# Performance work log

Hardware: AMD Instinct MI355X
Metric: run time of the kernel (lower is better)

The kernel has to match this reference:

```python
import jax, jax.numpy as jnp
import numpy as np
import math

B, S, E, H = 2, 2048, 1024, 16
D = E // H

def setup_inputs() -> dict:
    key = jax.random.key(0)
    ks = jax.random.split(key, 12)
    f = lambda k, shp: jax.random.normal(k, shp, dtype=jnp.float32)
    inp = {
        'Q': f(ks[0], (B, S, E)),
        'K': f(ks[1], (B, S, E)),
        'V': f(ks[2], (B, S, E)),
        # torch nn.Linear stores weight as [out, in]; y = x @ W.T + b
        'Wq': f(ks[3], (E, E)) * 0.02, 'bq': f(ks[4], (E,)) * 0.02,
        'Wk': f(ks[5], (E, E)) * 0.02, 'bk': f(ks[6], (E,)) * 0.02,
        'Wv': f(ks[7], (E, E)) * 0.02, 'bv': f(ks[8], (E,)) * 0.02,
        'Wo': f(ks[9], (E, E)) * 0.02, 'bo': f(ks[10], (E,)) * 0.02,
        # causal mask, broadcast over batch and heads: [1,1,S,S]
        'mask': jnp.tril(jnp.ones((S, S), dtype=jnp.int32))[None, None],
    }
    return inp

def reference(Q, K, V, Wq, bq, Wk, bk, Wv, bv, Wo, bo, mask):
    scale = 1.0 / math.sqrt(D)
    def proj(x, W, b):  # [B,S,E] -> [B,H,S,D]
        return (x @ W.T + b).reshape(B, S, H, D).transpose(0, 2, 1, 3)
    q = proj(Q, Wq, bq)
    k = proj(K, Wk, bk)
    v = proj(V, Wv, bv)
    scores = jnp.einsum('bhqd,bhkd->bhqk', q, k) * scale  # [B,H,S,S]
    scores = jnp.where(mask == 0, jnp.float32(-jnp.inf), scores)
    probs = jax.nn.softmax(scores, axis=-1)
    # dropout is identity in eval mode (deterministic reference)
    attn = jnp.einsum('bhqk,bhkd->bhqd', probs, v)
    attn = attn.transpose(0, 2, 1, 3).reshape(B, S, E)
    return attn @ Wo.T + bo
```

## Files before the change

### kernel.cpp

```cpp
#include <hip/hip_runtime.h>
#include <hip/hip_bf16.h>
#include <stdint.h>
#include <stddef.h>

#define S_LEN 2048
#define EMB   1024
#define NH    16
#define DH    64
#define BB    2
#define QBLK  64
#define NQT   (S_LEN / QBLK)

typedef short s16;
typedef __attribute__((ext_vector_type(8))) short bf16x8;
typedef __attribute__((ext_vector_type(4))) short s16x4;
typedef __attribute__((ext_vector_type(4))) float f32x4;

__device__ __forceinline__ float b2f(s16 x) {
  union { unsigned u; float f; } t;
  t.u = ((unsigned)(unsigned short)x) << 16;
  return t.f;
}
__device__ __forceinline__ s16 f2b(float f) {
  union { float f; unsigned u; } t;
  t.f = f;
  unsigned u = t.u;
  unsigned r = (u + 0x7FFFu + ((u >> 16) & 1u)) >> 16;
  return (s16)r;
}

__device__ __forceinline__ void gld16(const void* g, void* l) {
  __builtin_amdgcn_global_load_lds(
      (const __attribute__((address_space(1))) void*)g,
      (__attribute__((address_space(3))) void*)l, 16, 0, 0);
}
__device__ __forceinline__ void drain_and_barrier() {
  asm volatile("s_waitcnt vmcnt(0)" ::: "memory");
  __builtin_amdgcn_s_barrier();
}

struct CvtArgs { const float* src[11]; s16* dst[11]; int n[11]; };

__global__ __launch_bounds__(256)
void convert_in(CvtArgs a) {
  const int t = blockIdx.z;
  const int n = a.n[t];
  const int base = blockIdx.x * 2048 + threadIdx.x * 8;
  if (base >= n) return;
  const float* s = a.src[t] + base;
  float4 v0 = *(const float4*)s;
  float4 v1 = *(const float4*)(s + 4);
  bf16x8 o;
  o[0] = f2b(v0.x); o[1] = f2b(v0.y); o[2] = f2b(v0.z); o[3] = f2b(v0.w);
  o[4] = f2b(v1.x); o[5] = f2b(v1.y); o[6] = f2b(v1.z); o[7] = f2b(v1.w);
  *(bf16x8*)(a.dst[t] + base) = o;
}

struct GemmSet { const s16* X; const s16* W; const s16* Bv; s16* Y; float* Yf; int mode; };
struct GemmArgs { GemmSet t[3]; };

__global__ __launch_bounds__(256, 2)
void gemm_bt(GemmArgs args) {
  constexpr int K = EMB;
  constexpr int BK = 64;
  __shared__ __align__(16) s16 As[128][BK];
  __shared__ __align__(16) s16 Ws[128][BK];

  GemmSet p = args.t[blockIdx.z];
  const int tid  = threadIdx.x;
  const int lane = tid & 63;
  const int wave = tid >> 6;
  const int wr = wave >> 1, wc = wave & 1;
  const int l16 = lane & 15, lh = lane >> 4;
  const int brow = blockIdx.y * 128;
  const int bcol = blockIdx.x * 128;

  f32x4 acc[4][4] = {};

  for (int kt = 0; kt < K; kt += BK) {
#pragma unroll
    for (int r = 0; r < 4; ++r) {
      int cc = r * 256 + tid;
      int row = cc >> 3, col8 = (cc & 7) << 3;
      gld16(p.X + (size_t)(brow + row) * K + kt + col8, &As[row][col8]);
    }
#pragma unroll
    for (int r = 0; r < 4; ++r) {
      int cc = r * 256 + tid;
      int row = cc >> 3, col8 = (cc & 7) << 3;
      gld16(p.W + (size_t)(bcol + row) * K + kt + col8, &Ws[row][col8]);
    }
    __syncthreads();
#pragma unroll
    for (int kk = 0; kk < BK; kk += 32) {
      bf16x8 af[4], bfr[4];
#pragma unroll
      for (int i = 0; i < 4; ++i)
        af[i] = *(const bf16x8*)&As[wr * 64 + i * 16 + l16][kk + lh * 8];
#pragma unroll
      for (int j = 0; j < 4; ++j)
        bfr[j] = *(const bf16x8*)&Ws[wc * 64 + j * 16 + l16][kk + lh * 8];
#pragma unroll
      for (int i = 0; i < 4; ++i)
#pragma unroll
        for (int j = 0; j < 4; ++j)
          acc[i][j] = __builtin_amdgcn_mfma_f32_16x16x32_bf16(af[i], bfr[j], acc[i][j], 0, 0, 0);
    }
    __syncthreads();
  }

  const int mode = p.mode;
  float bv[4];
#pragma unroll
  for (int j = 0; j < 4; ++j) bv[j] = b2f(p.Bv[bcol + wc * 64 + j * 16 + l16]);
#pragma unroll
  for (int i = 0; i < 4; ++i) {
    int row0 = brow + wr * 64 + i * 16 + lh * 4;
#pragma unroll
    for (int j = 0; j < 4; ++j) {
      int col = bcol + wc * 64 + j * 16 + l16;
      if (mode == 2) {
        int bq = row0 >> 11, s0 = row0 & (S_LEN - 1);
        int hh = col >> 6, dd = col & 63;
        s16x4 pk;
#pragma unroll
        for (int t = 0; t < 4; ++t) pk[t] = f2b(acc[i][j][t] + bv[j]);
        *(s16x4*)&p.Y[(((size_t)bq * NH + hh) * DH + dd) * S_LEN + s0] = pk;
      } else {
#pragma unroll
        for (int t = 0; t < 4; ++t) {
          float v = acc[i][j][t] + bv[j];
          int r = row0 + t;
          if (mode == 0) {
            int bq = r >> 11, s = r & (S_LEN - 1);
            int hh = col >> 6, dd = col & 63;
            p.Y[((((size_t)bq * NH + hh) * S_LEN + s) << 6) + dd] = f2b(v);
          } else {
            p.Yf[(size_t)r * EMB + col] = v;
          }
        }
      }
    }
  }
}

__global__ __launch_bounds__(256, 3)
void attn_fwd(const s16* __restrict__ Qb, const s16* __restrict__ Kb,
              const s16* __restrict__ Vtb, s16* __restrict__ Ob) {
  __shared__ __align__(16) s16 Ks[2][4096];
  __shared__ __align__(16) s16 Vt[2][4096];
  __shared__ __align__(16) s16 Ps[4][16][68];

  const int tid  = threadIdx.x;
  const int lane = tid & 63;
  const int wave = tid >> 6;
  const int l16 = lane & 15, lh = lane >> 4;

  const int bid = blockIdx.x;
  const int xcd = bid & 7, slot = bid >> 3;
  const int bh = xcd * 4 + (slot >> 5);
  const int qi = (NQT - 1) - (slot & 31);
  const int qb = qi * QBLK;
  const int b = bh >> 4, h = bh & 15;

  const s16* Qp = Qb + (size_t)bh * S_LEN * DH;
  const s16* Kp = Kb + (size_t)bh * S_LEN * DH;
  const s16* Vp = Vtb + (size_t)bh * DH * S_LEN;

  auto stage_kv = [&](int kb, int bf) {
#pragma unroll
    for (int r = 0; r < 2; ++r) {
      int u = r * 256 + tid;
      int row = ((u >> 7) << 4) + (u & 15);
      int ch  = (((u >> 6) & 1) << 2) + ((u >> 4) & 3);
      gld16(Kp + (size_t)(kb + row) * DH + (ch << 3), &Ks[bf][(size_t)u * 8]);
    }
#pragma unroll
    for (int r = 0; r < 2; ++r) {
      int u = r * 256 + tid;
      int dv = ((u >> 7) << 4) + (u & 15);
      int ch = (((u >> 6) & 1) << 2) + ((u >> 4) & 3);
      gld16(Vp + (size_t)dv * S_LEN + kb + (ch << 3), &Vt[bf][(size_t)u * 8]);
    }
  };

  bf16x8 qf[2];
#pragma unroll
  for (int kk = 0; kk < 2; ++kk)
    qf[kk] = *(const bf16x8*)(Qp + (size_t)(qb + wave * 16 + l16) * DH + kk * 32 + lh * 8);

  stage_kv(0, 0);
  drain_and_barrier();

  float mrow[4], lrow[4];
  f32x4 accO[4] = {};
#pragma unroll
  for (int i = 0; i < 4; ++i) { mrow[i] = -1e30f; lrow[i] = 0.f; }

  int c = 0;
  for (int t = 0; t <= qi; ++t) {
    const int kb = t * QBLK;
    if (t < qi) stage_kv(kb + QBLK, c ^ 1);

    f32x4 sc[4] = {};
    __builtin_amdgcn_s_setprio(1);
#pragma unroll
    for (int kk = 0; kk < 2; ++kk) {
#pragma unroll
      for (int j = 0; j < 4; ++j) {
        bf16x8 kf = *(const bf16x8*)&Ks[c][(((j * 2 + kk) * 64) + lane) * 8];
        sc[j] = __builtin_amdgcn_mfma_f32_16x16x32_bf16(qf[kk], kf, sc[j], 0, 0, 0);
      }
    }
    __builtin_amdgcn_s_setprio(0);

    const bool diag = (t == qi);
    float pm[4];
#pragma unroll
    for (int i = 0; i < 4; ++i) {
#pragma unroll
      for (int j = 0; j < 4; ++j) {
        float s = sc[j][i] * 0.125f;
        if (diag && (kb + j * 16 + l16 > qb + wave * 16 + lh * 4 + i)) s = -1e30f;
        sc[j][i] = s;
      }
      pm[i] = fmaxf(fmaxf(sc[0][i], sc[1][i]), fmaxf(sc[2][i], sc[3][i]));
    }
#pragma unroll
    for (int d = 1; d < 16; d <<= 1)
#pragma unroll
      for (int i = 0; i < 4; ++i) pm[i] = fmaxf(pm[i], __shfl_xor(pm[i], d));
#pragma unroll
    for (int i = 0; i < 4; ++i) {
      float mnew = fmaxf(mrow[i], pm[i]);
      float corr = __expf(mrow[i] - mnew);
      mrow[i] = mnew;
      float rs = 0.f;
#pragma unroll
      for (int j = 0; j < 4; ++j) { float pv = __expf(sc[j][i] - mnew); sc[j][i] = pv; rs += pv; }
#pragma unroll
      for (int d = 1; d < 16; d <<= 1) rs += __shfl_xor(rs, d);
      lrow[i] = lrow[i] * corr + rs;
#pragma unroll
      for (int dc = 0; dc < 4; ++dc) accO[dc][i] *= corr;
    }

#pragma unroll
    for (int i = 0; i < 4; ++i)
#pragma unroll
      for (int j = 0; j < 4; ++j)
        Ps[wave][lh * 4 + i][j * 16 + l16] = f2b(sc[j][i]);

    bf16x8 pf[2];
#pragma unroll
    for (int kk = 0; kk < 2; ++kk) {
      const s16* pp = &Ps[wave][l16][kk * 32 + lh * 8];
      s16x4 lo = *(const s16x4*)pp;
      s16x4 hi = *(const s16x4*)(pp + 4);
      pf[kk] = __builtin_shufflevector(lo, hi, 0, 1, 2, 3, 4, 5, 6, 7);
    }
    __builtin_amdgcn_s_setprio(1);
#pragma unroll
    for (int kk = 0; kk < 2; ++kk) {
#pragma unroll
      for (int dc = 0; dc < 4; ++dc) {
        bf16x8 vf = *(const bf16x8*)&Vt[c][(((dc * 2 + kk) * 64) + lane) * 8];
        accO[dc] = __builtin_amdgcn_mfma_f32_16x16x32_bf16(pf[kk], vf, accO[dc], 0, 0, 0);
      }
    }
    __builtin_amdgcn_s_setprio(0);
    drain_and_barrier();
    c ^= 1;
  }

#pragma unroll
  for (int i = 0; i < 4; ++i) {
    float inv = 1.f / lrow[i];
    int srow = qb + wave * 16 + lh * 4 + i;
    size_t rowbase = ((size_t)b * S_LEN + srow) * EMB + h * DH;
#pragma unroll
    for (int dc = 0; dc < 4; ++dc)
      Ob[rowbase + dc * 16 + l16] = f2b(accO[dc][i] * inv);
  }
}

extern "C" void kernel_launch(void* const* d_in, const int* in_sizes, int n_in,
                              void* d_out, int out_size, void* d_ws, size_t ws_size,
                              hipStream_t stream) {
  const size_t NQ = (size_t)BB * S_LEN * EMB;
  const size_t NW = (size_t)EMB * EMB;
  const size_t NB2 = EMB;

  s16* Qc  = (s16*)d_ws;
  s16* Kc  = Qc + NQ;
  s16* Vc  = Kc + NQ;
  s16* Wqc = Vc + NQ;
  s16* Wkc = Wqc + NW;
  s16* Wvc = Wkc + NW;
  s16* Woc = Wvc + NW;
  s16* bqc = Woc + NW;
  s16* bkc = bqc + NB2;
  s16* bvc = bkc + NB2;
  s16* boc = bvc + NB2;
  s16* qw  = boc + NB2;
  s16* kw  = qw + NQ;
  s16* vw  = kw + NQ;
  s16* aw  = Qc;

  CvtArgs ca;
  const int srcmap[11] = {0, 1, 2, 3, 5, 7, 9, 4, 6, 8, 10};
  s16* dsts[11] = {Qc, Kc, Vc, Wqc, Wkc, Wvc, Woc, bqc, bkc, bvc, boc};
  for (int i = 0; i < 11; ++i) {
    ca.src[i] = (const float*)d_in[srcmap[i]];
    ca.dst[i] = dsts[i];
    ca.n[i]   = in_sizes[srcmap[i]];
  }
  convert_in<<<dim3(2048, 1, 11), 256, 0, stream>>>(ca);

  GemmArgs qkv;
  qkv.t[0] = {Qc, Wqc, bqc, qw, nullptr, 0};
  qkv.t[1] = {Kc, Wkc, bkc, kw, nullptr, 0};
  qkv.t[2] = {Vc, Wvc, bvc, vw, nullptr, 2};
  gemm_bt<<<dim3(8, 32, 3), 256, 0, stream>>>(qkv);

  attn_fwd<<<dim3(1024, 1), 256, 0, stream>>>(qw, kw, vw, aw);

  GemmArgs og;
  og.t[0] = {aw, Woc, boc, nullptr, (float*)d_out, 1};
  og.t[1] = og.t[0];
  og.t[2] = og.t[0];
  gemm_bt<<<dim3(8, 32, 1), 256, 0, stream>>>(og);
}
```

Before: 282.5 us.

## Transpose attention MFMA operands, keep P in registers, pair causal tiles per block

The attention kernel swaps the MFMA operand order (K as A, Q as B), so each lane holds a query column. The softmax reduction then needs only two cross-lane shuffles, and P is packed straight into bf16 MFMA fragments with v_cvt_pk_bf16_f32 instead of going through an LDS scratch tile. K is staged with a permuted row order to match the new fragment layout. Each block now handles a short and a long causal q-tile pair to balance work, with half as many blocks and occupancy hint 2. The 1/sqrt(D) scale is folded into the Q projection epilogue, which rounds the scaled value to bf16 earlier.

```diff
diff --git a/kernel.cpp b/kernel.cpp
--- a/kernel.cpp
+++ b/kernel.cpp
@@ -27,6 +27,11 @@
   unsigned u = t.u;
   unsigned r = (u + 0x7FFFu + ((u >> 16) & 1u)) >> 16;
   return (s16)r;
+}
+__device__ __forceinline__ unsigned cvtpk(float lo, float hi) {
+  unsigned r;
+  asm("v_cvt_pk_bf16_f32 %0, %1, %2" : "=v"(r) : "v"(lo), "v"(hi));
+  return r;
 }
 
 __device__ __forceinline__ void gld16(const void* g, void* l) {
@@ -56,7 +61,7 @@
   *(bf16x8*)(a.dst[t] + base) = o;
 }
 
-struct GemmSet { const s16* X; const s16* W; const s16* Bv; s16* Y; float* Yf; int mode; };
+struct GemmSet { const s16* X; const s16* W; const s16* Bv; s16* Y; float* Yf; float scale; int mode; };
 struct GemmArgs { GemmSet t[3]; };
 
 __global__ __launch_bounds__(256, 2)
@@ -110,6 +115,7 @@
   }
 
   const int mode = p.mode;
+  const float sc = p.scale;
   float bv[4];
 #pragma unroll
   for (int j = 0; j < 4; ++j) bv[j] = b2f(p.Bv[bcol + wc * 64 + j * 16 + l16]);
@@ -124,12 +130,12 @@
         int hh = col >> 6, dd = col & 63;
         s16x4 pk;
 #pragma unroll
-        for (int t = 0; t < 4; ++t) pk[t] = f2b(acc[i][j][t] + bv[j]);
+        for (int t = 0; t < 4; ++t) pk[t] = f2b((acc[i][j][t] + bv[j]) * sc);
         *(s16x4*)&p.Y[(((size_t)bq * NH + hh) * DH + dd) * S_LEN + s0] = pk;
       } else {
 #pragma unroll
         for (int t = 0; t < 4; ++t) {
-          float v = acc[i][j][t] + bv[j];
+          float v = (acc[i][j][t] + bv[j]) * sc;
           int r = row0 + t;
           if (mode == 0) {
             int bq = r >> 11, s = r & (S_LEN - 1);
@@ -144,12 +150,11 @@
   }
 }
 
-__global__ __launch_bounds__(256, 3)
+__global__ __launch_bounds__(256, 2)
 void attn_fwd(const s16* __restrict__ Qb, const s16* __restrict__ Kb,
               const s16* __restrict__ Vtb, s16* __restrict__ Ob) {
   __shared__ __align__(16) s16 Ks[2][4096];
   __shared__ __align__(16) s16 Vt[2][4096];
-  __shared__ __align__(16) s16 Ps[4][16][68];
 
   const int tid  = threadIdx.x;
   const int lane = tid & 63;
@@ -158,9 +163,8 @@
 
   const int bid = blockIdx.x;
   const int xcd = bid & 7, slot = bid >> 3;
-  const int bh = xcd * 4 + (slot >> 5);
-  const int qi = (NQT - 1) - (slot & 31);
-  const int qb = qi * QBLK;
+  const int bh = xcd * 4 + (slot >> 4);
+  const int qp = slot & 15;
   const int b = bh >> 4, h = bh & 15;
 
   const s16* Qp = Qb + (size_t)bh * S_LEN * DH;
@@ -171,9 +175,9 @@
 #pragma unroll
     for (int r = 0; r < 2; ++r) {
       int u = r * 256 + tid;
-      int row = ((u >> 7) << 4) + (u & 15);
-      int ch  = (((u >> 6) & 1) << 2) + ((u >> 4) & 3);
-      gld16(Kp + (size_t)(kb + row) * DH + (ch << 3), &Ks[bf][(size_t)u * 8]);
+      int rowp = ((u >> 8) & 1) * 32 + ((u >> 2) & 3) * 8 + ((u >> 7) & 1) * 4 + (u & 3);
+      int ch   = (((u >> 6) & 1) << 2) + ((u >> 4) & 3);
+      gld16(Kp + (size_t)(kb + rowp) * DH + (ch << 3), &Ks[bf][(size_t)u * 8]);
     }
 #pragma unroll
     for (int r = 0; r < 2; ++r) {
@@ -184,103 +188,105 @@
     }
   };
 
-  bf16x8 qf[2];
-#pragma unroll
-  for (int kk = 0; kk < 2; ++kk)
-    qf[kk] = *(const bf16x8*)(Qp + (size_t)(qb + wave * 16 + l16) * DH + kk * 32 + lh * 8);
-
-  stage_kv(0, 0);
-  drain_and_barrier();
-
-  float mrow[4], lrow[4];
-  f32x4 accO[4] = {};
-#pragma unroll
-  for (int i = 0; i < 4; ++i) { mrow[i] = -1e30f; lrow[i] = 0.f; }
-
-  int c = 0;
-  for (int t = 0; t <= qi; ++t) {
-    const int kb = t * QBLK;
-    if (t < qi) stage_kv(kb + QBLK, c ^ 1);
-
-    f32x4 sc[4] = {};
-    __builtin_amdgcn_s_setprio(1);
-#pragma unroll
-    for (int kk = 0; kk < 2; ++kk) {
-#pragma unroll
-      for (int j = 0; j < 4; ++j) {
-        bf16x8 kf = *(const bf16x8*)&Ks[c][(((j * 2 + kk) * 64) + lane) * 8];
-        sc[j] = __builtin_amdgcn_mfma_f32_16x16x32_bf16(qf[kk], kf, sc[j], 0, 0, 0);
+  for (int sel = 0; sel < 2; ++sel) {
+    const int qi = sel ? (NQT - 1 - qp) : qp;
+    const int qb = qi * QBLK;
+    const int q_glob = qb + wave * 16 + l16;
+
+    bf16x8 qf[2];
+#pragma unroll
+    for (int kk = 0; kk < 2; ++kk)
+      qf[kk] = *(const bf16x8*)(Qp + (size_t)q_glob * DH + kk * 32 + lh * 8);
+
+    stage_kv(0, 0);
+    drain_and_barrier();
+
+    float m = -1e30f, lsum = 0.f;
+    f32x4 accO[4] = {};
+
+    int c = 0;
+    for (int t = 0; t <= qi; ++t) {
+      const int kb = t * QBLK;
+      if (t < qi) stage_kv(kb + QBLK, c ^ 1);
+
+      f32x4 sc[4] = {};
+      __builtin_amdgcn_s_setprio(1);
+#pragma unroll
+      for (int kk = 0; kk < 2; ++kk) {
+#pragma unroll
+        for (int jb = 0; jb < 4; ++jb) {
+          bf16x8 kf = *(const bf16x8*)&Ks[c][(((jb * 2 + kk) * 64) + lane) * 8];
+          sc[jb] = __builtin_amdgcn_mfma_f32_16x16x32_bf16(kf, qf[kk], sc[jb], 0, 0, 0);
+        }
       }
-    }
-    __builtin_amdgcn_s_setprio(0);
-
-    const bool diag = (t == qi);
-    float pm[4];
-#pragma unroll
-    for (int i = 0; i < 4; ++i) {
-#pragma unroll
-      for (int j = 0; j < 4; ++j) {
-        float s = sc[j][i] * 0.125f;
-        if (diag && (kb + j * 16 + l16 > qb + wave * 16 + lh * 4 + i)) s = -1e30f;
-        sc[j][i] = s;
+      __builtin_amdgcn_s_setprio(0);
+
+      const int rel = q_glob - kb;
+      float pm = -1e30f;
+#pragma unroll
+      for (int jb = 0; jb < 4; ++jb)
+#pragma unroll
+        for (int r = 0; r < 4; ++r) {
+          int koff = ((jb >> 1) << 5) + (lh << 3) + ((jb & 1) << 2) + r;
+          float s = (koff <= rel) ? sc[jb][r] : -1e30f;
+          sc[jb][r] = s;
+          pm = fmaxf(pm, s);
+        }
+      pm = fmaxf(pm, __shfl_xor(pm, 16));
+      pm = fmaxf(pm, __shfl_xor(pm, 32));
+
+      float mnew = fmaxf(m, pm);
+      float corr = __expf(m - mnew);
+      m = mnew;
+      float rs = 0.f;
+#pragma unroll
+      for (int jb = 0; jb < 4; ++jb)
+#pragma unroll
+        for (int r = 0; r < 4; ++r) {
+          float pv = __expf(sc[jb][r] - mnew);
+          sc[jb][r] = pv;
+          rs += pv;
+        }
+      rs += __shfl_xor(rs, 16);
+      rs += __shfl_xor(rs, 32);
+      lsum = lsum * corr + rs;
+#pragma unroll
+      for (int dc = 0; dc < 4; ++dc) accO[dc] *= corr;
+
+      bf16x8 pf[2];
+#pragma unroll
+      for (int kk = 0; kk < 2; ++kk) {
+        union { unsigned u[4]; bf16x8 v; } pk;
+        pk.u[0] = cvtpk(sc[2 * kk][0], sc[2 * kk][1]);
+        pk.u[1] = cvtpk(sc[2 * kk][2], sc[2 * kk][3]);
+        pk.u[2] = cvtpk(sc[2 * kk + 1][0], sc[2 * kk + 1][1]);
+        pk.u[3] = cvtpk(sc[2 * kk + 1][2], sc[2 * kk + 1][3]);
+        pf[kk] = pk.v;
       }
-      pm[i] = fmaxf(fmaxf(sc[0][i], sc[1][i]), fmaxf(sc[2][i], sc[3][i]));
-    }
-#pragma unroll
-    for (int d = 1; d < 16; d <<= 1)
-#pragma unroll
-      for (int i = 0; i < 4; ++i) pm[i] = fmaxf(pm[i], __shfl_xor(pm[i], d));
-#pragma unroll
-    for (int i = 0; i < 4; ++i) {
-      float mnew = fmaxf(mrow[i], pm[i]);
-      float corr = __expf(mrow[i] - mnew);
-      mrow[i] = mnew;
-      float rs = 0.f;
-#pragma unroll
-      for (int j = 0; j < 4; ++j) { float pv = __expf(sc[j][i] - mnew); sc[j][i] = pv; rs += pv; }
-#pragma unroll
-      for (int d = 1; d < 16; d <<= 1) rs += __shfl_xor(rs, d);
-      lrow[i] = lrow[i] * corr + rs;
-#pragma unroll
-      for (int dc = 0; dc < 4; ++dc) accO[dc][i] *= corr;
-    }
-
-#pragma unroll
-    for (int i = 0; i < 4; ++i)
-#pragma unroll
-      for (int j = 0; j < 4; ++j)
-        Ps[wave][lh * 4 + i][j * 16 + l16] = f2b(sc[j][i]);
-
-    bf16x8 pf[2];
-#pragma unroll
-    for (int kk = 0; kk < 2; ++kk) {
-      const s16* pp = &Ps[wave][l16][kk * 32 + lh * 8];
-      s16x4 lo = *(const s16x4*)pp;
-      s16x4 hi = *(const s16x4*)(pp + 4);
-      pf[kk] = __builtin_shufflevector(lo, hi, 0, 1, 2, 3, 4, 5, 6, 7);
-    }
-    __builtin_amdgcn_s_setprio(1);
-#pragma unroll
-    for (int kk = 0; kk < 2; ++kk) {
-#pragma unroll
-      for (int dc = 0; dc < 4; ++dc) {
-        bf16x8 vf = *(const bf16x8*)&Vt[c][(((dc * 2 + kk) * 64) + lane) * 8];
-        accO[dc] = __builtin_amdgcn_mfma_f32_16x16x32_bf16(pf[kk], vf, accO[dc], 0, 0, 0);
+
+      __builtin_amdgcn_s_setprio(1);
+#pragma unroll
+      for (int kk = 0; kk < 2; ++kk) {
+#pragma unroll
+        for (int dc = 0; dc < 4; ++dc) {
+          bf16x8 vf = *(const bf16x8*)&Vt[c][(((dc * 2 + kk) * 64) + lane) * 8];
+          accO[dc] = __builtin_amdgcn_mfma_f32_16x16x32_bf16(vf, pf[kk], accO[dc], 0, 0, 0);
+        }
       }
-    }
-    __builtin_amdgcn_s_setprio(0);
-    drain_and_barrier();
-    c ^= 1;
-  }
-
-#pragma unroll
-  for (int i = 0; i < 4; ++i) {
-    float inv = 1.f / lrow[i];
-    int srow = qb + wave * 16 + lh * 4 + i;
-    size_t rowbase = ((size_t)b * S_LEN + srow) * EMB + h * DH;
-#pragma unroll
-    for (int dc = 0; dc < 4; ++dc)
-      Ob[rowbase + dc * 16 + l16] = f2b(accO[dc][i] * inv);
+      __builtin_amdgcn_s_setprio(0);
+      drain_and_barrier();
+      c ^= 1;
+    }
+
+    float inv = 1.f / lsum;
+    size_t rowbase = ((size_t)b * S_LEN + q_glob) * EMB + h * DH;
+#pragma unroll
+    for (int dc = 0; dc < 4; ++dc) {
+      s16x4 pk;
+#pragma unroll
+      for (int r = 0; r < 4; ++r) pk[r] = f2b(accO[dc][r] * inv);
+      *(s16x4*)&Ob[rowbase + dc * 16 + lh * 4] = pk;
+    }
   }
 }
 
@@ -318,15 +324,15 @@
   convert_in<<<dim3(2048, 1, 11), 256, 0, stream>>>(ca);
 
   GemmArgs qkv;
-  qkv.t[0] = {Qc, Wqc, bqc, qw, nullptr, 0};
-  qkv.t[1] = {Kc, Wkc, bkc, kw, nullptr, 0};
-  qkv.t[2] = {Vc, Wvc, bvc, vw, nullptr, 2};
+  qkv.t[0] = {Qc, Wqc, bqc, qw, nullptr, 0.125f, 0};
+  qkv.t[1] = {Kc, Wkc, bkc, kw, nullptr, 1.0f, 0};
+  qkv.t[2] = {Vc, Wvc, bvc, vw, nullptr, 1.0f, 2};
   gemm_bt<<<dim3(8, 32, 3), 256, 0, stream>>>(qkv);
 
-  attn_fwd<<<dim3(1024, 1), 256, 0, stream>>>(qw, kw, vw, aw);
+  attn_fwd<<<dim3(512, 1), 256, 0, stream>>>(qw, kw, vw, aw);
 
   GemmArgs og;
-  og.t[0] = {aw, Woc, boc, nullptr, (float*)d_out, 1};
+  og.t[0] = {aw, Woc, boc, nullptr, (float*)d_out, 1.0f, 1};
   og.t[1] = og.t[0];
   og.t[2] = og.t[0];
   gemm_bt<<<dim3(8, 32, 1), 256, 0, stream>>>(og);
```

New measurement: 246.0 us. 1.15x faster.
